# Optimization experiments

Hardware: AMD Instinct MI355X
Metric: run time of the kernel (lower is better)

The kernel has to match this reference:

```python
import jax, jax.numpy as jnp
import numpy as np

MIN_MZ, MAX_MZ, STEP = 0.0, 1000.0, 0.01
NUM_BINS = int((MAX_MZ - MIN_MZ) / STEP)      # 100000
GROUP_SIZE, OUT_PER_GROUP = 30, 3
GROUPS = NUM_BINS // GROUP_SIZE               # 3333
BINNER_OUT = GROUPS * OUT_PER_GROUP           # 9999
B, P = 256, 512


def setup_inputs() -> dict:
    key = jax.random.key(0)
    ks = jax.random.split(key, 16)
    mz1 = jax.random.uniform(ks[0], (B, P), jnp.float32) * 1000.0
    int1 = jax.random.uniform(ks[1], (B, P), jnp.float32)
    mz2 = jax.random.uniform(ks[2], (B, P), jnp.float32) * 1000.0
    int2 = jax.random.uniform(ks[3], (B, P), jnp.float32)

    def lin(k, fan_in, shape):
        return jax.random.normal(k, shape, jnp.float32) * (1.0 / np.sqrt(fan_in))

    Wg = lin(ks[4], GROUP_SIZE, (GROUPS, GROUP_SIZE, OUT_PER_GROUP))
    bg = jnp.zeros((GROUPS, OUT_PER_GROUP), jnp.float32)
    W1 = lin(ks[5], BINNER_OUT, (BINNER_OUT, 1000)); b1 = jnp.zeros((1000,), jnp.float32)
    W2 = lin(ks[6], 1000, (1000, 1000));             b2 = jnp.zeros((1000,), jnp.float32)
    W3 = lin(ks[7], 1000, (1000, 1000));             b3 = jnp.zeros((1000,), jnp.float32)
    Wo = lin(ks[8], 1000, (1000, 500));              bo = jnp.zeros((500,), jnp.float32)
    return {"mz1": mz1, "int1": int1, "mz2": mz2, "int2": int2,
            "Wg": Wg, "bg": bg, "W1": W1, "b1": b1, "W2": W2, "b2": b2,
            "W3": W3, "b3": b3, "Wo": Wo, "bo": bo}


def _bin_spectra(mz, inten):
    # histogram scatter-add: [B, P] peaks -> [B, NUM_BINS]
    idx = jnp.floor((mz - MIN_MZ) / STEP).astype(jnp.int32)
    valid = (mz >= MIN_MZ) & (mz < MAX_MZ)
    idx = jnp.clip(idx, 0, NUM_BINS - 1)
    vals = jnp.where(valid, inten, 0.0)
    out = jnp.zeros((mz.shape[0], NUM_BINS), inten.dtype)
    rows = jnp.arange(mz.shape[0])[:, None]
    return out.at[rows, idx].add(vals)


def _encode(mz, inten, Wg, bg, W1, b1, W2, b2, W3, b3, Wo, bo):
    x = _bin_spectra(mz, inten)                                # [B, NUM_BINS]
    xg = x[:, :GROUPS * GROUP_SIZE].reshape(-1, GROUPS, GROUP_SIZE)
    h = jnp.einsum('bgi,gio->bgo', xg, Wg) + bg                # grouped tiny linears
    h = h.reshape(-1, BINNER_OUT)
    h = jax.nn.relu(h @ W1 + b1)
    h = jax.nn.relu(h @ W2 + b2)
    h = jax.nn.relu(h @ W3 + b3)
    return h @ Wo + bo                                         # [B, 500]


def reference(mz1, int1, mz2, int2, Wg, bg, W1, b1, W2, b2, W3, b3, Wo, bo):
    e1 = _encode(mz1, int1, Wg, bg, W1, b1, W2, b2, W3, b3, Wo, bo)
    e2 = _encode(mz2, int2, Wg, bg, W1, b1, W2, b2, W3, b3, Wo, bo)
    eps = jnp.float32(1e-6)
    n1 = jnp.maximum(jnp.linalg.norm(e1, axis=1), eps)
    n2 = jnp.maximum(jnp.linalg.norm(e2, axis=1), eps)
    return jnp.sum(e1 * e2, axis=1) / (n1 * n2)
```

## Files before the change

### kernel.cpp

```cpp
#include <hip/hip_runtime.h>
#include <hip/hip_fp16.h>

using half8  = __attribute__((ext_vector_type(8))) _Float16;
using half4  = __attribute__((ext_vector_type(4))) _Float16;
using f32x4  = __attribute__((ext_vector_type(4))) float;

#define GROUPS      3333
#define BINNER_OUT  9999
#define BATCH       256
#define ROWS        512
#define PEAKS       512
#define K1          9999
#define K1P         10048
#define NP          1024
#define NOP         512
#define HALFK       5024

__device__ __forceinline__ void gl_lds16(const void* g, void* l) {
  __builtin_amdgcn_global_load_lds(
      (const __attribute__((address_space(1))) void*)g,
      (__attribute__((address_space(3))) void*)l, 16, 0, 0);
}

__device__ __forceinline__ void hs_add(float* p, float v) {
  __hip_atomic_fetch_add(p, v, __ATOMIC_RELAXED, __HIP_MEMORY_SCOPE_WORKGROUP);
}

__global__ __launch_bounds__(256) void prep5(
    const float* __restrict__ mz1, const float* __restrict__ it1,
    const float* __restrict__ mz2, const float* __restrict__ it2,
    const float* __restrict__ Wg,  const float* __restrict__ bg,
    _Float16* __restrict__ h16,
    const float* __restrict__ W1, _Float16* __restrict__ W1t,
    const float* __restrict__ W2, _Float16* __restrict__ W2t,
    const float* __restrict__ W3, _Float16* __restrict__ W3t,
    const float* __restrict__ Wo, _Float16* __restrict__ Wot) {
  __shared__ __align__(16) char smem[HALFK * 4];
  const int t = threadIdx.x;
  const int blk = blockIdx.x;

  if (blk < 1024) {
    float* hs = (float*)smem;
    const int row = blk >> 1, half = blk & 1;
    const int base = half * HALFK;
    const int s = row >> 8, b = row & 255;

    for (int k = t * 4; k < HALFK; k += 1024)
      *(f32x4*)&hs[k] = (f32x4){0.f, 0.f, 0.f, 0.f};
    __syncthreads();

    const float* mz = (s ? mz2 : mz1) + (size_t)b * PEAKS;
    const float* it = (s ? it2 : it1) + (size_t)b * PEAKS;

    float m[2], v[2], w[2][3]; int c0[2]; bool keep[2];
#pragma unroll
    for (int q = 0; q < 2; ++q) { m[q] = mz[t + q * 256]; v[q] = it[t + q * 256]; }
#pragma unroll
    for (int q = 0; q < 2; ++q) {
      bool val = (m[q] >= 0.0f && m[q] < 1000.0f);
      int bin = val ? (int)floorf(m[q] / 0.01f) : 0;
      bin = bin < 0 ? 0 : (bin > 99999 ? 99999 : bin);
      keep[q] = val && (bin < GROUPS * 30);
      int binL = bin < GROUPS * 30 ? bin : GROUPS * 30 - 1;
      const float* wp = Wg + (size_t)binL * 3;
      w[q][0] = wp[0]; w[q][1] = wp[1]; w[q][2] = wp[2];
      c0[q] = (bin / 30) * 3;
    }
#pragma unroll
    for (int q = 0; q < 2; ++q)
      if (keep[q]) {
#pragma unroll
        for (int o = 0; o < 3; ++o) {
          int c = c0[q] + o;
          if (c >= base && c < base + HALFK)
            hs_add(&hs[c - base], v[q] * w[q][o]);
        }
      }
    __syncthreads();

    _Float16* dst = h16 + (size_t)row * K1P + base;
    for (int k0 = t * 8; k0 < HALFK; k0 += 2048) {
      half8 vv;
#pragma unroll
      for (int j = 0; j < 8; ++j) {
        int c = base + k0 + j;
        float x = hs[k0 + j] + (c < BINNER_OUT ? bg[c] : 0.f);
        vv[j] = (_Float16)x;
      }
      *(half8*)(dst + k0) = vv;
    }
  } else {
    float* tf = (float*)smem;
    int bid = blk - 1024;
    const float* W; _Float16* outp; int K, N, Kpad, g, in, ktiles;
    if (bid < 640)       { W = W1; outp = W1t; K = K1;   N = 1000; Kpad = K1P;
                           ktiles = 157; g = bid % 40; in = bid / 40; }
    else if (bid < 704)  { bid -= 640; W = W2; outp = W2t; K = 1000; N = 1000;
                           Kpad = NP; ktiles = 16; g = bid & 3; in = bid >> 2; }
    else if (bid < 768)  { bid -= 704; W = W3; outp = W3t; K = 1000; N = 1000;
                           Kpad = NP; ktiles = 16; g = bid & 3; in = bid >> 2; }
    else                 { bid -= 768; W = Wo; outp = Wot; K = 1000; N = 500;
                           Kpad = NP; ktiles = 16; g = bid & 3; in = bid >> 2; }
    const int ntile = min(4, ktiles - g * 4);
    const int k0base = g * 256, n0 = in * 64;
    const int l = t & 63, wv = t >> 6;
    const int r = t >> 2, cc = (t & 3) * 16;
    const bool rok = (n0 + r < N);

    const int srow_l = l >> 4, scol = (l & 15) * 4;
    const int gnc = n0 + scol;
    const int gn = (gnc < N) ? gnc : 0;

    for (int i = 0; i < ntile; ++i) {
      const int k0 = k0base + i * 64;
#pragma unroll
      for (int j = 0; j < 4; ++j) {
        int gk = k0 + (wv * 4 + j) * 4 + srow_l;
        if (gk >= K) gk = K - 1;
        gl_lds16(W + (size_t)gk * N + gn, smem + (wv * 4 + j) * 1024);
      }
      __syncthreads();

#pragma unroll
      for (int h = 0; h < 2; ++h) {
        half8 v;
#pragma unroll
        for (int e = 0; e < 8; ++e) {
          int kk = cc + h * 8 + e;
          float x = (rok && (k0 + kk) < K) ? tf[kk * 64 + r] : 0.f;
          v[e] = (_Float16)x;
        }
        *(half8*)(outp + (size_t)(n0 + r) * Kpad + k0 + cc + h * 8) = v;
      }
      __syncthreads();
    }
  }
}

template <bool SWZ>
__global__ __launch_bounds__(256) void gemm_sk(
    const _Float16* __restrict__ A, int lda,
    const _Float16* __restrict__ Bt, int ldb,
    float* __restrict__ part, int M, int Npad, int ksteps_total, int kspc) {
  __shared__ __align__(16) _Float16 As[3 * 4096];
  __shared__ __align__(16) _Float16 Bs[3 * 8192];

  int bx, by, bz;
  if (SWZ) {
    int bid = blockIdx.x;
    int xcd = bid & 7, i = bid >> 3;
    bz = i >> 3;
    int j = i & 7;
    bx = (xcd & 3) * 2 + (j & 1);
    by = (xcd >> 2) * 4 + (j >> 1);
  } else {
    bx = blockIdx.x; by = blockIdx.y; bz = blockIdx.z;
  }

  const int t = threadIdx.x, lane = t & 63, wid = t >> 6;
  const int m0 = by * 64, n0 = bx * 128;
  const int s0 = bz * kspc;
  const int s1 = min(s0 + kspc, ksteps_total);

  const int wr = wid >> 1, wc = wid & 1;
  const int r16 = lane & 15, kh = lane >> 4;
  const int lr  = lane >> 3;
  const int lkc = ((lane & 7) ^ lr) * 8;
  const _Float16* AgL = A  + (size_t)(m0 + wid * 16 + lr) * lda + lkc;
  const _Float16* BgL = Bt + (size_t)(n0 + wid * 32 + lr) * ldb + lkc;

  f32x4 acc[2][4] = {};
  auto STAGE = [&](int s, int buf) {
    const size_t ko = (size_t)s * 64;
    _Float16* ab = As + buf * 4096 + wid * 1024;
    _Float16* bb = Bs + buf * 8192 + wid * 2048;
    gl_lds16(AgL + ko,                     ab);
    gl_lds16(AgL + ko + (size_t) 8 * lda,  ab + 512);
    gl_lds16(BgL + ko,                     bb);
    gl_lds16(BgL + ko + (size_t) 8 * ldb,  bb + 512);
    gl_lds16(BgL + ko + (size_t)16 * ldb,  bb + 1024);
    gl_lds16(BgL + ko + (size_t)24 * ldb,  bb + 1536);
  };

  if (s0 < s1)     STAGE(s0, 0);
  if (s0 + 1 < s1) STAGE(s0 + 1, 1);

  int cur = 0;
  for (int s = s0; s < s1; ++s) {
    __builtin_amdgcn_s_barrier();
    const bool more2 = (s + 2 < s1), more1 = (s + 1 < s1);
    if (more2) STAGE(s + 2, cur == 0 ? 2 : (cur == 1 ? 0 : 1));
    if (more2)      asm volatile("s_waitcnt vmcnt(12)" ::: "memory");
    else if (more1) asm volatile("s_waitcnt vmcnt(6)"  ::: "memory");
    else            asm volatile("s_waitcnt vmcnt(0)"  ::: "memory");
    __builtin_amdgcn_s_barrier();

    const char* Ab = (const char*)(As + cur * 4096);
    const char* Bb = (const char*)(Bs + cur * 8192);
    half8 af[2][2], bf[4][2];
#pragma unroll
    for (int kc = 0; kc < 2; ++kc) {
#pragma unroll
      for (int mi = 0; mi < 2; ++mi) {
        int row = wr * 32 + mi * 16 + r16;
        af[mi][kc] = *(const half8*)(Ab + row * 128 +
                     (((kc << 6) + (kh << 4)) ^ ((row & 7) << 4)));
      }
#pragma unroll
      for (int ni = 0; ni < 4; ++ni) {
        int row = wc * 64 + ni * 16 + r16;
        bf[ni][kc] = *(const half8*)(Bb + row * 128 +
                     (((kc << 6) + (kh << 4)) ^ ((row & 7) << 4)));
      }
    }
#pragma unroll
    for (int kc = 0; kc < 2; ++kc)
#pragma unroll
      for (int mi = 0; mi < 2; ++mi)
#pragma unroll
        for (int ni = 0; ni < 4; ++ni)
          acc[mi][ni] = __builtin_amdgcn_mfma_f32_16x16x32_f16(
              af[mi][kc], bf[ni][kc], acc[mi][ni], 0, 0, 0);
    cur = cur == 2 ? 0 : cur + 1;
  }

  float* P = part + (size_t)bz * M * Npad;
#pragma unroll
  for (int mi = 0; mi < 2; ++mi)
#pragma unroll
    for (int ni = 0; ni < 4; ++ni) {
      int row = m0 + wr * 32 + mi * 16 + kh * 4;
      int col = n0 + wc * 64 + ni * 16 + r16;
#pragma unroll
      for (int rr = 0; rr < 4; ++rr)
        P[(size_t)(row + rr) * Npad + col] = acc[mi][ni][rr];
    }
}

template <int RELU>
__global__ __launch_bounds__(256) void gemm_full(
    const _Float16* __restrict__ A,
    const _Float16* __restrict__ Bt,
    const float* __restrict__ bias, int Nreal, int Npad,
    _Float16* __restrict__ o16, float* __restrict__ o32) {
  __shared__ __align__(16) _Float16 As[3 * 4096];
  __shared__ __align__(16) _Float16 Bs[3 * 4096];

  const int bx = blockIdx.x, by = blockIdx.y;
  const int t = threadIdx.x, lane = t & 63, wid = t >> 6;
  const int m0 = by * 64, n0 = bx * 64;
  const int wr = wid >> 1, wc = wid & 1;
  const int r16 = lane & 15, kh = lane >> 4;
  const int lr  = lane >> 3;
  const int lkc = ((lane & 7) ^ lr) * 8;
  const _Float16* AgL = A  + (size_t)(m0 + wid * 16 + lr) * NP + lkc;
  const _Float16* BgL = Bt + (size_t)(n0 + wid * 16 + lr) * NP + lkc;

  f32x4 acc[2][2] = {};
  auto STAGE = [&](int s, int buf) {
    const size_t ko = (size_t)s * 64;
    _Float16* ab = As + buf * 4096 + wid * 1024;
    _Float16* bb = Bs + buf * 4096 + wid * 1024;
    gl_lds16(AgL + ko,                    ab);
    gl_lds16(AgL + ko + (size_t)8 * NP,   ab + 512);
    gl_lds16(BgL + ko,                    bb);
    gl_lds16(BgL + ko + (size_t)8 * NP,   bb + 512);
  };

  STAGE(0, 0);
  STAGE(1, 1);

  int cur = 0;
  for (int s = 0; s < 16; ++s) {
    __builtin_amdgcn_s_barrier();
    const bool more2 = (s + 2 < 16), more1 = (s + 1 < 16);
    if (more2) STAGE(s + 2, cur == 0 ? 2 : (cur == 1 ? 0 : 1));
    if (more2)      asm volatile("s_waitcnt vmcnt(8)" ::: "memory");
    else if (more1) asm volatile("s_waitcnt vmcnt(4)" ::: "memory");
    else            asm volatile("s_waitcnt vmcnt(0)" ::: "memory");
    __builtin_amdgcn_s_barrier();

    const char* Ab = (const char*)(As + cur * 4096);
    const char* Bb = (const char*)(Bs + cur * 4096);
    half8 af[2][2], bf[2][2];
#pragma unroll
    for (int kc = 0; kc < 2; ++kc) {
#pragma unroll
      for (int mi = 0; mi < 2; ++mi) {
        int row = wr * 32 + mi * 16 + r16;
        af[mi][kc] = *(const half8*)(Ab + row * 128 +
                     (((kc << 6) + (kh << 4)) ^ ((row & 7) << 4)));
      }
#pragma unroll
      for (int ni = 0; ni < 2; ++ni) {
        int row = wc * 32 + ni * 16 + r16;
        bf[ni][kc] = *(const half8*)(Bb + row * 128 +
                     (((kc << 6) + (kh << 4)) ^ ((row & 7) << 4)));
      }
    }
#pragma unroll
    for (int kc = 0; kc < 2; ++kc)
#pragma unroll
      for (int mi = 0; mi < 2; ++mi)
#pragma unroll
        for (int ni = 0; ni < 2; ++ni)
          acc[mi][ni] = __builtin_amdgcn_mfma_f32_16x16x32_f16(
              af[mi][kc], bf[ni][kc], acc[mi][ni], 0, 0, 0);
    cur = cur == 2 ? 0 : cur + 1;
  }

#pragma unroll
  for (int mi = 0; mi < 2; ++mi)
#pragma unroll
    for (int ni = 0; ni < 2; ++ni) {
      int row = m0 + wr * 32 + mi * 16 + kh * 4;
      int col = n0 + wc * 32 + ni * 16 + r16;
      float bb = (col < Nreal) ? bias[col] : 0.f;
#pragma unroll
      for (int rr = 0; rr < 4; ++rr) {
        float x = acc[mi][ni][rr] + bb;
        if (RELU) x = fmaxf(x, 0.f);
        if (o16) o16[(size_t)(row + rr) * Npad + col] = (_Float16)x;
        else     o32[(size_t)(row + rr) * Npad + col] = x;
      }
    }
}

__global__ void combine_sk(const float* __restrict__ part, int SK, int M, int Npad,
                           const float* __restrict__ bias, int Nreal,
                           _Float16* __restrict__ o16) {
  int i4 = (blockIdx.x * 256 + threadIdx.x) * 4;
  int total = M * Npad;
  if (i4 >= total) return;
  f32x4 s = (f32x4){0.f, 0.f, 0.f, 0.f};
  for (int zz = 0; zz < SK; ++zz)
    s += *(const f32x4*)&part[(size_t)zz * total + i4];
  int n = i4 & (Npad - 1);
  half4 v;
#pragma unroll
  for (int e = 0; e < 4; ++e) {
    float x = s[e] + ((n + e) < Nreal ? bias[n + e] : 0.f);
    v[e] = (_Float16)fmaxf(x, 0.f);
  }
  *(half4*)(o16 + i4) = v;
}

__global__ void cosine_E(const float* __restrict__ E, float* __restrict__ out) {
  const int b = blockIdx.x, t = threadIdx.x;
  float d = 0.f, s1 = 0.f, s2 = 0.f;
  for (int c = t; c < NOP; c += 256) {
    float e1 = E[(size_t)b * NOP + c];
    float e2 = E[(size_t)(b + BATCH) * NOP + c];
    d += e1 * e2; s1 += e1 * e1; s2 += e2 * e2;
  }
  for (int off = 32; off > 0; off >>= 1) {
    d  += __shfl_down(d, off, 64);
    s1 += __shfl_down(s1, off, 64);
    s2 += __shfl_down(s2, off, 64);
  }
  __shared__ float rd[4], r1[4], r2[4];
  int wd = t >> 6, lane = t & 63;
  if (lane == 0) { rd[wd] = d; r1[wd] = s1; r2[wd] = s2; }
  __syncthreads();
  if (t == 0) {
    float D  = rd[0] + rd[1] + rd[2] + rd[3];
    float S1 = r1[0] + r1[1] + r1[2] + r1[3];
    float S2 = r2[0] + r2[1] + r2[2] + r2[3];
    float n1 = fmaxf(sqrtf(S1), 1e-6f);
    float n2 = fmaxf(sqrtf(S2), 1e-6f);
    out[b] = D / (n1 * n2);
  }
}

extern "C" void kernel_launch(void* const* d_in, const int* in_sizes, int n_in,
                              void* d_out, int out_size, void* d_ws, size_t ws_size,
                              hipStream_t stream) {
  const float* mz1 = (const float*)d_in[0];
  const float* it1 = (const float*)d_in[1];
  const float* mz2 = (const float*)d_in[2];
  const float* it2 = (const float*)d_in[3];
  const float* Wg  = (const float*)d_in[4];
  const float* bg  = (const float*)d_in[5];
  const float* W1  = (const float*)d_in[6];
  const float* b1  = (const float*)d_in[7];
  const float* W2  = (const float*)d_in[8];
  const float* b2  = (const float*)d_in[9];
  const float* W3  = (const float*)d_in[10];
  const float* b3  = (const float*)d_in[11];
  const float* Wo  = (const float*)d_in[12];
  const float* bo  = (const float*)d_in[13];
  float* out = (float*)d_out;

  char* ws = (char*)d_ws;
  size_t off = 0;
  auto take = [&](size_t bytes) {
    size_t o = off; off += (bytes + 255) & ~(size_t)255; return o;
  };
  float*    part = (float*)   (ws + take((size_t)8 * ROWS * NP * 4));
  _Float16* h16  = (_Float16*)(ws + take((size_t)ROWS * K1P * 2));
  _Float16* W1t  = (_Float16*)(ws + take((size_t)NP * K1P * 2));
  _Float16* W2t  = (_Float16*)(ws + take((size_t)NP * NP * 2));
  _Float16* W3t  = (_Float16*)(ws + take((size_t)NP * NP * 2));
  _Float16* Wot  = (_Float16*)(ws + take((size_t)NOP * NP * 2));
  _Float16* y1   = (_Float16*)(ws + take((size_t)ROWS * NP * 2));
  _Float16* y2   = (_Float16*)(ws + take((size_t)ROWS * NP * 2));
  _Float16* y3   = (_Float16*)(ws + take((size_t)ROWS * NP * 2));
  float*    E    = (float*)   (ws + take((size_t)ROWS * NOP * 4));

  prep5<<<1824, 256, 0, stream>>>(mz1, it1, mz2, it2, Wg, bg, h16,
                                  W1, W1t, W2, W2t, W3, W3t, Wo, Wot);

  gemm_sk<true><<<512, 256, 0, stream>>>(
      h16, K1P, W1t, K1P, part, ROWS, NP, K1P / 64, 20);
  combine_sk<<<(ROWS * NP) / 1024, 256, 0, stream>>>(part, 8, ROWS, NP, b1, 1000, y1);

  gemm_full<1><<<dim3(NP / 64, ROWS / 64), 256, 0, stream>>>(
      y1, W2t, b2, 1000, NP, y2, nullptr);
  gemm_full<1><<<dim3(NP / 64, ROWS / 64), 256, 0, stream>>>(
      y2, W3t, b3, 1000, NP, y3, nullptr);
  gemm_full<0><<<dim3(NOP / 64, ROWS / 64), 256, 0, stream>>>(
      y3, Wot, bo, 500, NOP, nullptr, E);

  cosine_E<<<BATCH, 256, 0, stream>>>(E, out);
}
```

Baseline: 88.13 us.

## Deepen split-K GEMM pipeline to six stages with 32-wide K steps

Restructures the first split-K GEMM so each stage loads a 32-wide K slice instead of 64 and keeps five stages in flight instead of two, using six LDS buffers. The XOR swizzle and load mapping change to match the narrower rows, and the vmcnt waits are recalculated for the deeper queue. The aim is to hide global-memory latency on the large W1 operand. In exchange there are twice as many barriers per unit of K and fewer MFMAs between synchronisations.

```diff
diff --git a/kernel.cpp b/kernel.cpp
--- a/kernel.cpp
+++ b/kernel.cpp
@@ -142,8 +142,8 @@
     const _Float16* __restrict__ A, int lda,
     const _Float16* __restrict__ Bt, int ldb,
     float* __restrict__ part, int M, int Npad, int ksteps_total, int kspc) {
-  __shared__ __align__(16) _Float16 As[3 * 4096];
-  __shared__ __align__(16) _Float16 Bs[3 * 8192];
+  __shared__ __align__(16) _Float16 As[6 * 2048];
+  __shared__ __align__(16) _Float16 Bs[6 * 4096];
 
   int bx, by, bz;
   if (SWZ) {
@@ -164,64 +164,61 @@
 
   const int wr = wid >> 1, wc = wid & 1;
   const int r16 = lane & 15, kh = lane >> 4;
-  const int lr  = lane >> 3;
-  const int lkc = ((lane & 7) ^ lr) * 8;
-  const _Float16* AgL = A  + (size_t)(m0 + wid * 16 + lr) * lda + lkc;
-  const _Float16* BgL = Bt + (size_t)(n0 + wid * 32 + lr) * ldb + lkc;
+
+  const int srA = wid * 16 + (lane >> 2);
+  const int scA = (((lane & 3) ^ (srA & 3)) * 8);
+  const int srB = wid * 32 + (lane >> 2);
+  const int scB = (((lane & 3) ^ (srB & 3)) * 8);
+  const _Float16* AgL = A  + (size_t)(m0 + srA) * lda + scA;
+  const _Float16* BgL = Bt + (size_t)(n0 + srB) * ldb + scB;
 
   f32x4 acc[2][4] = {};
   auto STAGE = [&](int s, int buf) {
-    const size_t ko = (size_t)s * 64;
-    _Float16* ab = As + buf * 4096 + wid * 1024;
-    _Float16* bb = Bs + buf * 8192 + wid * 2048;
-    gl_lds16(AgL + ko,                     ab);
-    gl_lds16(AgL + ko + (size_t) 8 * lda,  ab + 512);
-    gl_lds16(BgL + ko,                     bb);
-    gl_lds16(BgL + ko + (size_t) 8 * ldb,  bb + 512);
-    gl_lds16(BgL + ko + (size_t)16 * ldb,  bb + 1024);
-    gl_lds16(BgL + ko + (size_t)24 * ldb,  bb + 1536);
+    const size_t ko = (size_t)s * 32;
+    gl_lds16(AgL + ko,                     As + buf * 2048 + wid * 512);
+    gl_lds16(BgL + ko,                     Bs + buf * 4096 + wid * 1024);
+    gl_lds16(BgL + ko + (size_t)16 * ldb,  Bs + buf * 4096 + wid * 1024 + 512);
   };
 
-  if (s0 < s1)     STAGE(s0, 0);
-  if (s0 + 1 < s1) STAGE(s0 + 1, 1);
+#pragma unroll
+  for (int i = 0; i < 5; ++i)
+    if (s0 + i < s1) STAGE(s0 + i, i);
 
   int cur = 0;
   for (int s = s0; s < s1; ++s) {
     __builtin_amdgcn_s_barrier();
-    const bool more2 = (s + 2 < s1), more1 = (s + 1 < s1);
-    if (more2) STAGE(s + 2, cur == 0 ? 2 : (cur == 1 ? 0 : 1));
-    if (more2)      asm volatile("s_waitcnt vmcnt(12)" ::: "memory");
-    else if (more1) asm volatile("s_waitcnt vmcnt(6)"  ::: "memory");
-    else            asm volatile("s_waitcnt vmcnt(0)"  ::: "memory");
+    int ahead = s1 - 1 - s; ahead = ahead > 5 ? 5 : ahead;
+    if (ahead == 5) STAGE(s + 5, cur >= 1 ? cur - 1 : cur + 5);
+    switch (ahead) {
+      case 5:  asm volatile("s_waitcnt vmcnt(15)" ::: "memory"); break;
+      case 4:  asm volatile("s_waitcnt vmcnt(12)" ::: "memory"); break;
+      case 3:  asm volatile("s_waitcnt vmcnt(9)"  ::: "memory"); break;
+      case 2:  asm volatile("s_waitcnt vmcnt(6)"  ::: "memory"); break;
+      case 1:  asm volatile("s_waitcnt vmcnt(3)"  ::: "memory"); break;
+      default: asm volatile("s_waitcnt vmcnt(0)"  ::: "memory"); break;
+    }
     __builtin_amdgcn_s_barrier();
 
-    const char* Ab = (const char*)(As + cur * 4096);
-    const char* Bb = (const char*)(Bs + cur * 8192);
-    half8 af[2][2], bf[4][2];
-#pragma unroll
-    for (int kc = 0; kc < 2; ++kc) {
-#pragma unroll
-      for (int mi = 0; mi < 2; ++mi) {
-        int row = wr * 32 + mi * 16 + r16;
-        af[mi][kc] = *(const half8*)(Ab + row * 128 +
-                     (((kc << 6) + (kh << 4)) ^ ((row & 7) << 4)));
-      }
-#pragma unroll
-      for (int ni = 0; ni < 4; ++ni) {
-        int row = wc * 64 + ni * 16 + r16;
-        bf[ni][kc] = *(const half8*)(Bb + row * 128 +
-                     (((kc << 6) + (kh << 4)) ^ ((row & 7) << 4)));
-      }
-    }
-#pragma unroll
-    for (int kc = 0; kc < 2; ++kc)
-#pragma unroll
-      for (int mi = 0; mi < 2; ++mi)
-#pragma unroll
-        for (int ni = 0; ni < 4; ++ni)
-          acc[mi][ni] = __builtin_amdgcn_mfma_f32_16x16x32_f16(
-              af[mi][kc], bf[ni][kc], acc[mi][ni], 0, 0, 0);
-    cur = cur == 2 ? 0 : cur + 1;
+    const char* Ab = (const char*)(As + cur * 2048);
+    const char* Bb = (const char*)(Bs + cur * 4096);
+    half8 af[2], bf[4];
+#pragma unroll
+    for (int mi = 0; mi < 2; ++mi) {
+      int row = wr * 32 + mi * 16 + r16;
+      af[mi] = *(const half8*)(Ab + row * 64 + ((kh ^ (row & 3)) << 4));
+    }
+#pragma unroll
+    for (int ni = 0; ni < 4; ++ni) {
+      int row = wc * 64 + ni * 16 + r16;
+      bf[ni] = *(const half8*)(Bb + row * 64 + ((kh ^ (row & 3)) << 4));
+    }
+#pragma unroll
+    for (int mi = 0; mi < 2; ++mi)
+#pragma unroll
+      for (int ni = 0; ni < 4; ++ni)
+        acc[mi][ni] = __builtin_amdgcn_mfma_f32_16x16x32_f16(
+            af[mi], bf[ni], acc[mi][ni], 0, 0, 0);
+    cur = cur == 5 ? 0 : cur + 1;
   }
 
   float* P = part + (size_t)bz * M * Npad;
@@ -411,7 +408,7 @@
                                   W1, W1t, W2, W2t, W3, W3t, Wo, Wot);
 
   gemm_sk<true><<<512, 256, 0, stream>>>(
-      h16, K1P, W1t, K1P, part, ROWS, NP, K1P / 64, 20);
+      h16, K1P, W1t, K1P, part, ROWS, NP, K1P / 32, 40);
   combine_sk<<<(ROWS * NP) / 1024, 256, 0, stream>>>(part, 8, ROWS, NP, b1, 1000, y1);
 
   gemm_full<1><<<dim3(NP / 64, ROWS / 64), 256, 0, stream>>>(
```

After: 94.53 us. 7.3% more time.
